# Kernel tuning notes

Measured on AMD Instinct MI355X. Metric: run time of the kernel, lower is better.

The kernel has to match this reference:

```python
import jax, jax.numpy as jnp
import numpy as np

B, T, I, H, O = 128, 512, 128, 256, 1

def setup_inputs() -> dict:
    key = jax.random.key(0)
    ks = jax.random.split(key, 7)
    s_ih = 1.0 / np.sqrt(H)
    return {
        "x": jax.random.normal(ks[0], (B, T, I), dtype=jnp.float32),
        "W_ih": jax.random.uniform(ks[1], (H, I), minval=-s_ih, maxval=s_ih, dtype=jnp.float32),
        "W_hh": jax.random.uniform(ks[2], (H, H), minval=-s_ih, maxval=s_ih, dtype=jnp.float32),
        "b_ih": jax.random.uniform(ks[3], (H,), minval=-s_ih, maxval=s_ih, dtype=jnp.float32),
        "b_hh": jax.random.uniform(ks[4], (H,), minval=-s_ih, maxval=s_ih, dtype=jnp.float32),
        "W_fc": jax.random.uniform(ks[5], (O, H), minval=-s_ih, maxval=s_ih, dtype=jnp.float32),
        "b_fc": jax.random.uniform(ks[6], (O,), minval=-s_ih, maxval=s_ih, dtype=jnp.float32),
    }

def reference(x, W_ih, W_hh, b_ih, b_hh, W_fc, b_fc):
    # Precompute input projections for all timesteps: [B, T, H]
    xp = jnp.einsum("bti,hi->bth", x, W_ih) + b_ih + b_hh
    h0 = jnp.zeros((x.shape[0], W_hh.shape[0]), dtype=x.dtype)

    def step(h, xp_t):
        h_new = jnp.tanh(xp_t + h @ W_hh.T)
        return h_new, None

    # scan over time axis; only final hidden state is needed
    h_last, _ = jax.lax.scan(step, h0, jnp.swapaxes(xp, 0, 1))
    logits = h_last @ W_fc.T + b_fc
    return jax.nn.sigmoid(logits)
```

## Files before the change

kernel.cpp:

```cpp
#include <hip/hip_runtime.h>
#include <hip/hip_bf16.h>


#define B_ 128
#define T_ 512
#define I_ 128
#define H_ 256
#define SCALE 2.8853900817779268f

typedef __attribute__((ext_vector_type(8))) short short8;
typedef __attribute__((ext_vector_type(4))) float floatx4;

__device__ __forceinline__ short8 pack8(float4 lo, float4 hi) {
    __hip_bfloat162 p0 = __float22bfloat162_rn(float2{lo.x, lo.y});
    __hip_bfloat162 p1 = __float22bfloat162_rn(float2{lo.z, lo.w});
    __hip_bfloat162 p2 = __float22bfloat162_rn(float2{hi.x, hi.y});
    __hip_bfloat162 p3 = __float22bfloat162_rn(float2{hi.z, hi.w});
    int4 i;
    i.x = *(int*)&p0; i.y = *(int*)&p1; i.z = *(int*)&p2; i.w = *(int*)&p3;
    return *(short8*)&i;
}
__device__ __forceinline__ short8 pack8s(float4 lo, float4 hi, float s) {
    lo.x *= s; lo.y *= s; lo.z *= s; lo.w *= s;
    hi.x *= s; hi.y *= s; hi.z *= s; hi.w *= s;
    return pack8(lo, hi);
}
__device__ __forceinline__ float tanh_s(float v) {
    float e = __builtin_amdgcn_exp2f(v);
    float r = __builtin_amdgcn_rcpf(e + 1.0f);
    return __builtin_fmaf(-2.0f, r, 1.0f);
}

__global__ __launch_bounds__(512, 2)
void rnn_fused(const float* __restrict__ x, const float* __restrict__ W_ih,
               const float* __restrict__ W_hh, const float* __restrict__ b_ih,
               const float* __restrict__ b_hh, const float* __restrict__ W_fc,
               const float* __restrict__ b_fc, float* __restrict__ out) {
    __shared__ __align__(16) short hbuf[2][16][256];
    __shared__ __align__(16) short xbuf[2][16][128];
    const int tid  = threadIdx.x;
    const int wave = tid >> 6, lane = tid & 63;
    const int l15  = lane & 15, quad = lane >> 4;
    const int b0   = blockIdx.x * 16;
    const int n0   = wave * 32;
    const int swz  = l15 & 7;

    short8 wfrag[2][8];
#pragma unroll
    for (int mt = 0; mt < 2; ++mt)
#pragma unroll
        for (int kq = 0; kq < 8; ++kq) {
            const float* p = W_hh + (long)(n0 + mt * 16 + l15) * H_ + kq * 32 + quad * 8;
            wfrag[mt][kq] = pack8s(*(const float4*)p, *(const float4*)(p + 4), SCALE);
        }
    short8 wih[2][4];
#pragma unroll
    for (int mt = 0; mt < 2; ++mt)
#pragma unroll
        for (int kq = 0; kq < 4; ++kq) {
            const float* p = W_ih + (long)(n0 + mt * 16 + l15) * I_ + kq * 32 + quad * 8;
            wih[mt][kq] = pack8s(*(const float4*)p, *(const float4*)(p + 4), SCALE);
        }
    floatx4 bias2[2];
#pragma unroll
    for (int mt = 0; mt < 2; ++mt)
#pragma unroll
        for (int r = 0; r < 4; ++r) {
            int n = n0 + mt * 16 + quad * 4 + r;
            bias2[mt][r] = SCALE * (b_ih[n] + b_hh[n]);
        }

    {
        int* hz = (int*)&hbuf[0][0][0];
#pragma unroll
        for (int i = tid; i < 16 * 256 / 2; i += 512) hz[i] = 0;
    }

    const int sb = tid >> 5, sj = tid & 31;
    const float* xsrc = x + (long)(b0 + sb) * T_ * I_ + sj * 4;
    const int xwoff = sb * 128 + ((sj ^ ((sb & 7) << 1)) << 2);
    {
        float4 s1 = *(const float4*)(xsrc + I_);
        __hip_bfloat162 q0 = __float22bfloat162_rn(float2{s1.x, s1.y});
        __hip_bfloat162 q1 = __float22bfloat162_rn(float2{s1.z, s1.w});
        int2 sw; sw.x = *(int*)&q0; sw.y = *(int*)&q1;
        *(int2*)(&xbuf[1][0][0] + xwoff) = sw;
    }
    float4 xhA = *(const float4*)(xsrc + 2 * I_);
    float4 xhB;

    int roff[8];
#pragma unroll
    for (int kq = 0; kq < 8; ++kq)
        roff[kq] = l15 * 256 + (((quad + 4 * kq) ^ swz) << 3);
    int xroff[4];
#pragma unroll
    for (int kq = 0; kq < 4; ++kq)
        xroff[kq] = l15 * 128 + (((kq * 4 + quad) ^ swz) << 3);
    int woff[2];
#pragma unroll
    for (int mt = 0; mt < 2; ++mt) {
        int c = wave * 4 + 2 * mt + (quad >> 1);
        woff[mt] = l15 * 256 + ((c ^ swz) << 3) + (quad & 1) * 4;
    }

    floatx4 aA[2], aB[2];
    {
        short8 xf[4];
#pragma unroll
        for (int kq = 0; kq < 4; ++kq) {
            const float* p = x + (long)(b0 + l15) * T_ * I_ + kq * 32 + quad * 8;
            xf[kq] = pack8(*(const float4*)p, *(const float4*)(p + 4));
        }
#pragma unroll
        for (int mt = 0; mt < 2; ++mt) aA[mt] = bias2[mt];
#pragma unroll
        for (int kq = 0; kq < 4; ++kq)
#pragma unroll
            for (int mt = 0; mt < 2; ++mt)
                aA[mt] = __builtin_amdgcn_mfma_f32_16x16x32_bf16(
                    wih[mt][kq], xf[kq], aA[mt], 0, 0, 0);
    }
    __syncthreads();

    const short* hb0r = &hbuf[0][0][0]; short* hb0w = &hbuf[0][0][0];
    const short* hb1r = &hbuf[1][0][0]; short* hb1w = &hbuf[1][0][0];
    const short* xb0r = &xbuf[0][0][0]; short* xb0w = &xbuf[0][0][0];
    const short* xb1r = &xbuf[1][0][0]; short* xb1w = &xbuf[1][0][0];

#define BAR() asm volatile("s_waitcnt lgkmcnt(0)\n\ts_barrier" ::: "memory")

#define STEP(HR, HW, XR, XW, ACUR, ANXT, XH, XN, TLD)                           \
    {                                                                           \
                 \
        XN = *(const float4*)(xsrc + (long)(TLD) * I_);                         \
                                                       \
        short8 hfrag[8];                                                        \
        _Pragma("unroll")                                                       \
        for (int kq = 0; kq < 8; ++kq)                                          \
            hfrag[kq] = *(const short8*)((HR) + roff[kq]);                      \
                             \
        floatx4 aZ[2];                                                          \
        _Pragma("unroll")                                                       \
        for (int mt = 0; mt < 2; ++mt) aZ[mt] = (floatx4){0.f, 0.f, 0.f, 0.f};  \
        _Pragma("unroll")                                                       \
        for (int kq = 0; kq < 4; ++kq)                                          \
            _Pragma("unroll")                                                   \
            for (int mt = 0; mt < 2; ++mt) {                                    \
                ACUR[mt] = __builtin_amdgcn_mfma_f32_16x16x32_bf16(             \
                    wfrag[mt][kq], hfrag[kq], ACUR[mt], 0, 0, 0);               \
                aZ[mt] = __builtin_amdgcn_mfma_f32_16x16x32_bf16(               \
                    wfrag[mt][kq + 4], hfrag[kq + 4], aZ[mt], 0, 0, 0);         \
            }                                                                   \
        \
        short8 xfrag[4];                                                        \
        _Pragma("unroll")                                                       \
        for (int kq = 0; kq < 4; ++kq)                                          \
            xfrag[kq] = *(const short8*)((XR) + xroff[kq]);                     \
        {                                                                       \
            __hip_bfloat162 q0 = __float22bfloat162_rn(float2{XH.x, XH.y});     \
            __hip_bfloat162 q1 = __float22bfloat162_rn(float2{XH.z, XH.w});     \
            int2 sw; sw.x = *(int*)&q0; sw.y = *(int*)&q1;                      \
            *(int2*)((XW) + xwoff) = sw;                                        \
        }                                                                       \
        \
        _Pragma("unroll")                                                       \
        for (int mt = 0; mt < 2; ++mt) {                                        \
            float r0 = tanh_s(ACUR[mt][0] + aZ[mt][0]);                         \
            float r1 = tanh_s(ACUR[mt][1] + aZ[mt][1]);                         \
            float r2 = tanh_s(ACUR[mt][2] + aZ[mt][2]);                         \
            float r3 = tanh_s(ACUR[mt][3] + aZ[mt][3]);                         \
            __hip_bfloat162 q01 = __float22bfloat162_rn(float2{r0, r1});        \
            __hip_bfloat162 q23 = __float22bfloat162_rn(float2{r2, r3});        \
            int2 wv; wv.x = *(int*)&q01; wv.y = *(int*)&q23;                    \
            *(int2*)((HW) + woff[mt]) = wv;                                     \
        }                                                                       \
                                   \
        _Pragma("unroll")                                                       \
        for (int mt = 0; mt < 2; ++mt) ANXT[mt] = bias2[mt];                    \
        _Pragma("unroll")                                                       \
        for (int kq = 0; kq < 4; ++kq)                                          \
            _Pragma("unroll")                                                   \
            for (int mt = 0; mt < 2; ++mt)                                      \
                ANXT[mt] = __builtin_amdgcn_mfma_f32_16x16x32_bf16(             \
                    wih[mt][kq], xfrag[kq], ANXT[mt], 0, 0, 0);                 \
        BAR();                                                                  \
    }

#pragma unroll 1
    for (int t = 0; t < T_; t += 2) {
        const int tl0 = (t + 3 < T_) ? t + 3 : T_ - 1;
        const int tl1 = (t + 4 < T_) ? t + 4 : T_ - 1;
        STEP(hb0r, hb1w, xb1r, xb0w, aA, aB, xhA, xhB, tl0);
        STEP(hb1r, hb0w, xb0r, xb1w, aB, aA, xhB, xhA, tl1);
    }
#undef STEP
#undef BAR

    if (tid < 256) {
        const int bl = tid >> 4, seg = tid & 15;
        const int bswz = bl & 7;
        float p = 0.0f;
#pragma unroll
        for (int half = 0; half < 2; ++half) {
            const int c = 2 * seg + half;
            const short* hr = &hbuf[0][0][0] + bl * 256 + ((c ^ bswz) << 3);
#pragma unroll
            for (int i = 0; i < 8; ++i) {
                __hip_bfloat16 hv = *(const __hip_bfloat16*)(hr + i);
                p += __bfloat162float(hv) * W_fc[c * 8 + i];
            }
        }
#pragma unroll
        for (int off = 1; off < 16; off <<= 1) p += __shfl_xor(p, off);
        if (seg == 0) out[b0 + bl] = 1.0f / (1.0f + __expf(-(p + b_fc[0])));
    }
}

extern "C" void kernel_launch(void* const* d_in, const int* in_sizes, int n_in,
                              void* d_out, int out_size, void* d_ws, size_t ws_size,
                              hipStream_t stream) {
    const float* x    = (const float*)d_in[0];
    const float* W_ih = (const float*)d_in[1];
    const float* W_hh = (const float*)d_in[2];
    const float* b_ih = (const float*)d_in[3];
    const float* b_hh = (const float*)d_in[4];
    const float* W_fc = (const float*)d_in[5];
    const float* b_fc = (const float*)d_in[6];
    float* out = (float*)d_out;
    (void)d_ws; (void)ws_size;

    rnn_fused<<<B_ / 16, 512, 0, stream>>>(x, W_ih, W_hh, b_ih, b_hh, W_fc, b_fc, out);
}
```

Baseline: 414.8 us.

## Split input projection into a separate parallel GEMM kernel before recurrence

Moves the x·W_ih projection out of the sequential recurrence into a standalone kernel that runs across 256 blocks and writes fp32 projections to workspace. The recurrent kernel then only loads the precomputed values per step, taking the input MFMAs, LDS staging and bf16 conversion off its critical path. In exchange it adds a second launch and roughly 64MB of global write and read traffic for the projection buffer, and it relies on the workspace being large enough.

```diff
diff --git a/kernel.cpp b/kernel.cpp
--- a/kernel.cpp
+++ b/kernel.cpp
@@ -31,13 +31,86 @@
     return __builtin_fmaf(-2.0f, r, 1.0f);
 }
 
+#define XP_GRID 256
+#define XP_NT   ((B_ * T_ / 16) / XP_GRID)
+__global__ __launch_bounds__(256, 1)
+void xp_kernel(const float* __restrict__ x, const float* __restrict__ W_ih,
+               const float* __restrict__ b_ih, const float* __restrict__ b_hh,
+               float* __restrict__ xp) {
+    const int tid  = threadIdx.x;
+    const int wave = tid >> 6, lane = tid & 63;
+    const int l15  = lane & 15, quad = lane >> 4;
+    const int n0   = wave * 64;
+
+    short8 wfrag[4][4];
+#pragma unroll
+    for (int mtt = 0; mtt < 4; ++mtt)
+#pragma unroll
+        for (int kq = 0; kq < 4; ++kq) {
+            const float* p = W_ih + (long)(n0 + mtt * 16 + l15) * I_ + kq * 32 + quad * 8;
+            wfrag[mtt][kq] = pack8s(*(const float4*)p, *(const float4*)(p + 4), SCALE);
+        }
+    floatx4 biasv[4];
+#pragma unroll
+    for (int mtt = 0; mtt < 4; ++mtt)
+#pragma unroll
+        for (int r = 0; r < 4; ++r) {
+            int n = n0 + mtt * 16 + quad * 4 + r;
+            biasv[mtt][r] = SCALE * (b_ih[n] + b_hh[n]);
+        }
+
+    const long mbase = (long)blockIdx.x * XP_NT * 16;
+
+    float4 qa[4][2], qb[4][2];
+#define LDX(Q, IT)                                                              \
+    {                                                                           \
+        const int itc = ((IT) < XP_NT) ? (IT) : (XP_NT - 1);                    \
+        const float* p = x + (mbase + (long)itc * 16 + l15) * I_ + quad * 8;    \
+        _Pragma("unroll")                                                       \
+        for (int kq = 0; kq < 4; ++kq) {                                        \
+            Q[kq][0] = *(const float4*)(p + kq * 32);                           \
+            Q[kq][1] = *(const float4*)(p + kq * 32 + 4);                       \
+        }                                                                       \
+    }
+#define ITER(Q, IT, ILD)                                                        \
+    {                                                                           \
+        short8 xf[4];                                                           \
+        _Pragma("unroll")                                                       \
+        for (int kq = 0; kq < 4; ++kq) xf[kq] = pack8(Q[kq][0], Q[kq][1]);      \
+        LDX(Q, ILD);                                                            \
+        floatx4 acc[4];                                                         \
+        _Pragma("unroll")                                                       \
+        for (int mtt = 0; mtt < 4; ++mtt) acc[mtt] = biasv[mtt];                \
+        _Pragma("unroll")                                                       \
+        for (int kq = 0; kq < 4; ++kq)                                          \
+            _Pragma("unroll")                                                   \
+            for (int mtt = 0; mtt < 4; ++mtt)                                   \
+                acc[mtt] = __builtin_amdgcn_mfma_f32_16x16x32_bf16(             \
+                    wfrag[mtt][kq], xf[kq], acc[mtt], 0, 0, 0);                 \
+        float* o = xp + (mbase + (long)(IT) * 16 + l15) * H_ + n0 + quad * 4;   \
+        _Pragma("unroll")                                                       \
+        for (int mtt = 0; mtt < 4; ++mtt) {                                     \
+            float4 st = {acc[mtt][0], acc[mtt][1], acc[mtt][2], acc[mtt][3]};   \
+            *(float4*)(o + mtt * 16) = st;                                      \
+        }                                                                       \
+    }
+
+    LDX(qa, 0);
+    LDX(qb, 1);
+#pragma unroll 1
+    for (int it = 0; it < XP_NT; it += 2) {
+        ITER(qa, it, it + 2);
+        ITER(qb, it + 1, it + 3);
+    }
+#undef ITER
+#undef LDX
+}
+
 __global__ __launch_bounds__(512, 2)
-void rnn_fused(const float* __restrict__ x, const float* __restrict__ W_ih,
-               const float* __restrict__ W_hh, const float* __restrict__ b_ih,
-               const float* __restrict__ b_hh, const float* __restrict__ W_fc,
-               const float* __restrict__ b_fc, float* __restrict__ out) {
+void rnn_kernel(const float* __restrict__ xp, const float* __restrict__ W_hh,
+                const float* __restrict__ W_fc, const float* __restrict__ b_fc,
+                float* __restrict__ out) {
     __shared__ __align__(16) short hbuf[2][16][256];
-    __shared__ __align__(16) short xbuf[2][16][128];
     const int tid  = threadIdx.x;
     const int wave = tid >> 6, lane = tid & 63;
     const int l15  = lane & 15, quad = lane >> 4;
@@ -53,22 +126,6 @@
             const float* p = W_hh + (long)(n0 + mt * 16 + l15) * H_ + kq * 32 + quad * 8;
             wfrag[mt][kq] = pack8s(*(const float4*)p, *(const float4*)(p + 4), SCALE);
         }
-    short8 wih[2][4];
-#pragma unroll
-    for (int mt = 0; mt < 2; ++mt)
-#pragma unroll
-        for (int kq = 0; kq < 4; ++kq) {
-            const float* p = W_ih + (long)(n0 + mt * 16 + l15) * I_ + kq * 32 + quad * 8;
-            wih[mt][kq] = pack8s(*(const float4*)p, *(const float4*)(p + 4), SCALE);
-        }
-    floatx4 bias2[2];
-#pragma unroll
-    for (int mt = 0; mt < 2; ++mt)
-#pragma unroll
-        for (int r = 0; r < 4; ++r) {
-            int n = n0 + mt * 16 + quad * 4 + r;
-            bias2[mt][r] = SCALE * (b_ih[n] + b_hh[n]);
-        }
 
     {
         int* hz = (int*)&hbuf[0][0][0];
@@ -76,27 +133,10 @@
         for (int i = tid; i < 16 * 256 / 2; i += 512) hz[i] = 0;
     }
 
-    const int sb = tid >> 5, sj = tid & 31;
-    const float* xsrc = x + (long)(b0 + sb) * T_ * I_ + sj * 4;
-    const int xwoff = sb * 128 + ((sj ^ ((sb & 7) << 1)) << 2);
-    {
-        float4 s1 = *(const float4*)(xsrc + I_);
-        __hip_bfloat162 q0 = __float22bfloat162_rn(float2{s1.x, s1.y});
-        __hip_bfloat162 q1 = __float22bfloat162_rn(float2{s1.z, s1.w});
-        int2 sw; sw.x = *(int*)&q0; sw.y = *(int*)&q1;
-        *(int2*)(&xbuf[1][0][0] + xwoff) = sw;
-    }
-    float4 xhA = *(const float4*)(xsrc + 2 * I_);
-    float4 xhB;
-
     int roff[8];
 #pragma unroll
     for (int kq = 0; kq < 8; ++kq)
         roff[kq] = l15 * 256 + (((quad + 4 * kq) ^ swz) << 3);
-    int xroff[4];
-#pragma unroll
-    for (int kq = 0; kq < 4; ++kq)
-        xroff[kq] = l15 * 128 + (((kq * 4 + quad) ^ swz) << 3);
     int woff[2];
 #pragma unroll
     for (int mt = 0; mt < 2; ++mt) {
@@ -104,95 +144,66 @@
         woff[mt] = l15 * 256 + ((c ^ swz) << 3) + (quad & 1) * 4;
     }
 
-    floatx4 aA[2], aB[2];
-    {
-        short8 xf[4];
-#pragma unroll
-        for (int kq = 0; kq < 4; ++kq) {
-            const float* p = x + (long)(b0 + l15) * T_ * I_ + kq * 32 + quad * 8;
-            xf[kq] = pack8(*(const float4*)p, *(const float4*)(p + 4));
-        }
-#pragma unroll
-        for (int mt = 0; mt < 2; ++mt) aA[mt] = bias2[mt];
-#pragma unroll
-        for (int kq = 0; kq < 4; ++kq)
-#pragma unroll
-            for (int mt = 0; mt < 2; ++mt)
-                aA[mt] = __builtin_amdgcn_mfma_f32_16x16x32_bf16(
-                    wih[mt][kq], xf[kq], aA[mt], 0, 0, 0);
-    }
+    const float* xpl = xp + (long)(b0 + l15) * T_ * H_ + n0 + quad * 4;
+    float4 xvA0 = *(const float4*)(xpl);
+    float4 xvA1 = *(const float4*)(xpl + 16);
+    float4 xvB0 = *(const float4*)(xpl + H_);
+    float4 xvB1 = *(const float4*)(xpl + H_ + 16);
+
     __syncthreads();
 
     const short* hb0r = &hbuf[0][0][0]; short* hb0w = &hbuf[0][0][0];
     const short* hb1r = &hbuf[1][0][0]; short* hb1w = &hbuf[1][0][0];
-    const short* xb0r = &xbuf[0][0][0]; short* xb0w = &xbuf[0][0][0];
-    const short* xb1r = &xbuf[1][0][0]; short* xb1w = &xbuf[1][0][0];
 
 #define BAR() asm volatile("s_waitcnt lgkmcnt(0)\n\ts_barrier" ::: "memory")
 
-#define STEP(HR, HW, XR, XW, ACUR, ANXT, XH, XN, TLD)                           \
+#define STEP(HR, HW, XV0, XV1, TLD)                                             \
     {                                                                           \
-                 \
-        XN = *(const float4*)(xsrc + (long)(TLD) * I_);                         \
-                                                       \
+                \
         short8 hfrag[8];                                                        \
         _Pragma("unroll")                                                       \
         for (int kq = 0; kq < 8; ++kq)                                          \
             hfrag[kq] = *(const short8*)((HR) + roff[kq]);                      \
+                      \
+        floatx4 aC[2], aZ[2];                                                   \
+        aC[0] = (floatx4){XV0.x, XV0.y, XV0.z, XV0.w};                          \
+        aC[1] = (floatx4){XV1.x, XV1.y, XV1.z, XV1.w};                          \
+        aZ[0] = (floatx4){0.f, 0.f, 0.f, 0.f};                                  \
+        aZ[1] = (floatx4){0.f, 0.f, 0.f, 0.f};                                  \
+            \
+        XV0 = *(const float4*)(xpl + (long)(TLD) * H_);                         \
+        XV1 = *(const float4*)(xpl + (long)(TLD) * H_ + 16);                    \
                              \
-        floatx4 aZ[2];                                                          \
-        _Pragma("unroll")                                                       \
-        for (int mt = 0; mt < 2; ++mt) aZ[mt] = (floatx4){0.f, 0.f, 0.f, 0.f};  \
         _Pragma("unroll")                                                       \
         for (int kq = 0; kq < 4; ++kq)                                          \
             _Pragma("unroll")                                                   \
             for (int mt = 0; mt < 2; ++mt) {                                    \
-                ACUR[mt] = __builtin_amdgcn_mfma_f32_16x16x32_bf16(             \
-                    wfrag[mt][kq], hfrag[kq], ACUR[mt], 0, 0, 0);               \
+                aC[mt] = __builtin_amdgcn_mfma_f32_16x16x32_bf16(               \
+                    wfrag[mt][kq], hfrag[kq], aC[mt], 0, 0, 0);                 \
                 aZ[mt] = __builtin_amdgcn_mfma_f32_16x16x32_bf16(               \
                     wfrag[mt][kq + 4], hfrag[kq + 4], aZ[mt], 0, 0, 0);         \
             }                                                                   \
-        \
-        short8 xfrag[4];                                                        \
-        _Pragma("unroll")                                                       \
-        for (int kq = 0; kq < 4; ++kq)                                          \
-            xfrag[kq] = *(const short8*)((XR) + xroff[kq]);                     \
-        {                                                                       \
-            __hip_bfloat162 q0 = __float22bfloat162_rn(float2{XH.x, XH.y});     \
-            __hip_bfloat162 q1 = __float22bfloat162_rn(float2{XH.z, XH.w});     \
-            int2 sw; sw.x = *(int*)&q0; sw.y = *(int*)&q1;                      \
-            *(int2*)((XW) + xwoff) = sw;                                        \
-        }                                                                       \
-        \
+               \
         _Pragma("unroll")                                                       \
         for (int mt = 0; mt < 2; ++mt) {                                        \
-            float r0 = tanh_s(ACUR[mt][0] + aZ[mt][0]);                         \
-            float r1 = tanh_s(ACUR[mt][1] + aZ[mt][1]);                         \
-            float r2 = tanh_s(ACUR[mt][2] + aZ[mt][2]);                         \
-            float r3 = tanh_s(ACUR[mt][3] + aZ[mt][3]);                         \
+            float r0 = tanh_s(aC[mt][0] + aZ[mt][0]);                           \
+            float r1 = tanh_s(aC[mt][1] + aZ[mt][1]);                           \
+            float r2 = tanh_s(aC[mt][2] + aZ[mt][2]);                           \
+            float r3 = tanh_s(aC[mt][3] + aZ[mt][3]);                           \
             __hip_bfloat162 q01 = __float22bfloat162_rn(float2{r0, r1});        \
             __hip_bfloat162 q23 = __float22bfloat162_rn(float2{r2, r3});        \
             int2 wv; wv.x = *(int*)&q01; wv.y = *(int*)&q23;                    \
             *(int2*)((HW) + woff[mt]) = wv;                                     \
         }                                                                       \
-                                   \
-        _Pragma("unroll")                                                       \
-        for (int mt = 0; mt < 2; ++mt) ANXT[mt] = bias2[mt];                    \
-        _Pragma("unroll")                                                       \
-        for (int kq = 0; kq < 4; ++kq)                                          \
-            _Pragma("unroll")                                                   \
-            for (int mt = 0; mt < 2; ++mt)                                      \
-                ANXT[mt] = __builtin_amdgcn_mfma_f32_16x16x32_bf16(             \
-                    wih[mt][kq], xfrag[kq], ANXT[mt], 0, 0, 0);                 \
         BAR();                                                                  \
     }
 
 #pragma unroll 1
     for (int t = 0; t < T_; t += 2) {
-        const int tl0 = (t + 3 < T_) ? t + 3 : T_ - 1;
-        const int tl1 = (t + 4 < T_) ? t + 4 : T_ - 1;
-        STEP(hb0r, hb1w, xb1r, xb0w, aA, aB, xhA, xhB, tl0);
-        STEP(hb1r, hb0w, xb0r, xb1w, aB, aA, xhB, xhA, tl1);
+        const int tl0 = (t + 2 < T_) ? t + 2 : T_ - 1;
+        const int tl1 = (t + 3 < T_) ? t + 3 : T_ - 1;
+        STEP(hb0r, hb1w, xvA0, xvA1, tl0);
+        STEP(hb1r, hb0w, xvB0, xvB1, tl1);
     }
 #undef STEP
 #undef BAR
@@ -228,7 +239,9 @@
     const float* W_fc = (const float*)d_in[5];
     const float* b_fc = (const float*)d_in[6];
     float* out = (float*)d_out;
-    (void)d_ws; (void)ws_size;
-
-    rnn_fused<<<B_ / 16, 512, 0, stream>>>(x, W_ih, W_hh, b_ih, b_hh, W_fc, b_fc, out);
-}
+
+    float* xp = (float*)d_ws;
+
+    xp_kernel<<<XP_GRID, 256, 0, stream>>>(x, W_ih, b_ih, b_hh, xp);
+    rnn_kernel<<<B_ / 16, 512, 0, stream>>>(xp, W_hh, W_fc, b_fc, out);
+}
```

After: 424.9 us. 2.4% more time.
